# Performance work log

Measured on AMD Instinct MI355X. Metric: run time of the kernel, lower is better.

Reference implementation:

```python
import jax, jax.numpy as jnp
import numpy as np

LATENT_CH = 64  # feature_ch // 8


def conv1x1(x, w):
    # Conv2dLayer with kernel_size=1, bias=False, activation='linear':
    # weight_gain = 1/sqrt(in_channels * 1)
    gain = 1.0 / np.sqrt(w.shape[1])
    return jnp.einsum('bchw,oc->bohw', x, w * gain)


def casual_attention(q, k, v):
    # q,k,v: [B, C, N] / [B, C, M]; score = q^T k, softmax over keys, out = score @ v^T
    score = jnp.einsum('bcn,bcm->bnm', q, k)
    score = jax.nn.softmax(score, axis=-1)
    return jnp.einsum('bnm,bcm->bnc', score, v)  # [B, N, C]


def reference(feature_map, concepts, w_theta, w_phi, w_g, w_o, gamma_sa, gamma_moca):
    B, C, H, W = feature_map.shape
    L = LATENT_CH
    HW = H * W

    # ---- SelfAttention ----
    th = conv1x1(feature_map, w_theta).reshape(B, L, HW)
    ph = conv1x1(feature_map, w_phi).reshape(B, L, HW)
    g = conv1x1(feature_map, w_g).reshape(B, L, HW)
    # torch does .view(-1, L, H, W) on a [B, HW, L] tensor -> raw memory reinterpret
    lat = casual_attention(th, ph, g).reshape(B, L, H, W)
    sa_out = gamma_sa * conv1x1(lat, w_o) + feature_map

    # ---- MomentumConceptAttention (theta and o shared with SA, trainable_conv=False) ----
    enc = conv1x1(sa_out, w_theta).reshape(B, L, HW)
    phi_c = concepts.T[None]                      # [1, L, P]  (torch.no_grad on concepts)
    phi_c = jnp.broadcast_to(phi_c, (B, L, concepts.shape[0]))
    lat2 = casual_attention(enc, phi_c, phi_c).reshape(B, L, H, W)
    out = gamma_moca * conv1x1(lat2, w_o) + sa_out
    return out


def setup_inputs() -> dict:
    key = jax.random.key(0)
    ks = jax.random.split(key, 8)
    B, C, H, W = 8, 512, 64, 64
    L, P = LATENT_CH, 256
    return {
        'feature_map': jax.random.normal(ks[0], (B, C, H, W), jnp.float32),
        'concepts': jax.random.normal(ks[1], (P, L), jnp.float32),
        'w_theta': jax.random.normal(ks[2], (L, C), jnp.float32),
        'w_phi': jax.random.normal(ks[3], (L, C), jnp.float32),
        'w_g': jax.random.normal(ks[4], (L, C), jnp.float32),
        'w_o': jax.random.normal(ks[5], (C, L), jnp.float32),
        'gamma_sa': jnp.float32(0.1),
        'gamma_moca': jnp.float32(0.1),
    }
```

## Files before the change

### kernel.cpp

```cpp
#include <hip/hip_runtime.h>
#include <math.h>

#define HW   4096
#define CINP 512
#define LCH  64

typedef short bf8 __attribute__((ext_vector_type(8)));
typedef float f4  __attribute__((ext_vector_type(4)));
typedef unsigned int u32x2 __attribute__((ext_vector_type(2)));

__device__ __forceinline__ unsigned short f2bf(float x) {
    union { float f; unsigned int u; } v; v.f = x;
    return (unsigned short)((v.u + 0x7fffu + ((v.u >> 16) & 1u)) >> 16);
}
__device__ __forceinline__ bf8 ldbf8(const unsigned short* p) {
    uint4 u = *(const uint4*)p;
    return __builtin_bit_cast(bf8, u);
}
__device__ __forceinline__ unsigned int cvtpk(float a, float b) {
    unsigned int r;
    asm volatile("v_cvt_pk_bf16_f32 %0, %1, %2" : "=v"(r) : "v"(a), "v"(b));
    return r;
}

__global__ __launch_bounds__(256) void precast(
    const float* __restrict__ wt, const float* __restrict__ wp,
    const float* __restrict__ wg, const float* __restrict__ wo,
    const float* __restrict__ conc,
    unsigned short* __restrict__ WB, unsigned short* __restrict__ WO,
    unsigned short* __restrict__ CK, unsigned short* __restrict__ CV)
{
    const float gain = 0.04419417382415922f;
    int id = blockIdx.x * 256 + threadIdx.x;
    if (id < 98304) {
        int o = id >> 9, k = id & 511;
        const float* w = (o < 64) ? wt : (o < 128) ? wp : wg;
        WB[id] = f2bf(w[(o & 63) * 512 + k] * gain);
    } else if (id < 131072) {
        int j = id - 98304;
        WO[j] = f2bf(wo[j]);
    } else if (id < 147456) {
        int j = id - 131072;
        CK[j] = f2bf(conc[j]);
    } else if (id < 163840) {
        int j = id - 147456;
        int l = j >> 8, m = j & 255;
        CV[j] = f2bf(conc[m * 64 + l]);
    }
}

__global__ __launch_bounds__(256) void cast_transpose(const float* __restrict__ x,
                                                      unsigned short* __restrict__ XT)
{
    __shared__ unsigned short Lb[64][72];
    const int t  = threadIdx.x;
    const int n0 = blockIdx.x * 64, c0 = blockIdx.y * 64, b = blockIdx.z;
    const float* xb = x + ((size_t)b * CINP + c0) * HW + n0;
    const int cc = t >> 4, n4 = (t & 15) * 4;
    #pragma unroll
    for (int i = 0; i < 4; i++) {
        int c = cc + i * 16;
        float4 v = *(const float4*)(xb + (size_t)c * HW + n4);
        Lb[n4 + 0][c] = f2bf(v.x);
        Lb[n4 + 1][c] = f2bf(v.y);
        Lb[n4 + 2][c] = f2bf(v.z);
        Lb[n4 + 3][c] = f2bf(v.w);
    }
    __syncthreads();
    const int n = t & 63, cb0 = t >> 6;
    unsigned short* orow = XT + ((size_t)b * HW + n0 + n) * CINP + c0;
    #pragma unroll
    for (int i = 0; i < 2; i++) {
        int cb = cb0 + i * 4;
        *(uint4*)(orow + cb * 8) = *(const uint4*)&Lb[n][cb * 8];
    }
}

__global__ __launch_bounds__(256) void lat_transpose(const unsigned short* __restrict__ A,
                                                     unsigned short* __restrict__ LT)
{
    __shared__ unsigned short Ls[64][72];
    const int t = threadIdx.x, s0 = blockIdx.x * 64, b = blockIdx.y;
    const unsigned short* ab = A + (size_t)b * LCH * HW;
    #pragma unroll
    for (int it = 0; it < 2; it++) {
        int c = (t >> 3) + it * 32, s8 = (t & 7) * 8;
        union { uint4 u; unsigned short s[8]; } v;
        v.u = *(const uint4*)(ab + (size_t)c * HW + s0 + s8);
        #pragma unroll
        for (int i = 0; i < 8; i++) Ls[s8 + i][c] = v.s[i];
    }
    __syncthreads();
    unsigned short* ob = LT + ((size_t)b * HW + s0) * LCH;
    #pragma unroll
    for (int it = 0; it < 2; it++) {
        int s = (t >> 3) + it * 32, c8 = (t & 7);
        *(uint4*)(ob + (size_t)s * LCH + c8 * 8) = *(const uint4*)&Ls[s][c8 * 8];
    }
}

template <int NRT>
__global__ __launch_bounds__(256) void qkv_gemm(unsigned short* XT,
                                                const unsigned short* __restrict__ WB,
                                                unsigned short* __restrict__ VL)
{
    const int t = threadIdx.x;
    const int wave = t >> 6, lane = t & 63, quad = lane >> 4, lidx = lane & 15;
    const int b = blockIdx.y;
    const int ncol = blockIdx.x * 64 + wave * 16 + lidx;
    unsigned short* xrow = XT + ((size_t)b * HW + ncol) * CINP;

    f4 acc[NRT];
    #pragma unroll
    for (int r = 0; r < NRT; r++) acc[r] = (f4){0.f, 0.f, 0.f, 0.f};

    for (int kk = 0; kk < 16; kk++) {
        const int k0 = kk * 32 + quad * 8;
        bf8 bq = ldbf8(xrow + k0);
        #pragma unroll
        for (int rt = 0; rt < NRT; rt++) {
            bf8 aw = ldbf8(WB + (size_t)(rt * 16 + lidx) * CINP + k0);
            acc[rt] = __builtin_amdgcn_mfma_f32_16x16x32_bf16(aw, bq, acc[rt], 0, 0, 0);
        }
    }

    #pragma unroll
    for (int rt = 0; rt < NRT; rt++) {
        if (rt < 8) {
            union { unsigned short s[4]; uint2 u; } pk;
            #pragma unroll
            for (int r = 0; r < 4; r++) pk.s[r] = f2bf(acc[rt][r]);
            int off = (rt < 4) ? (rt * 16 + quad * 4) : (64 + (rt - 4) * 16 + quad * 4);
            *(uint2*)(xrow + off) = pk.u;
        } else {
            #pragma unroll
            for (int r = 0; r < 4; r++) {
                int l = (rt - 8) * 16 + quad * 4 + r;
                VL[((size_t)b * LCH + l) * HW + ncol] = f2bf(acc[rt][r]);
            }
        }
    }
}

__global__ __launch_bounds__(128) void flash(
    const unsigned short* Qb, size_t qbat,
    const unsigned short* Kb, size_t krow, size_t kbat,
    const unsigned short* Vb, size_t vrow, size_t vbat,
    unsigned short* __restrict__ Aout, int nkeys)
{
    __shared__ __align__(16) unsigned short Ks[2][32][72];
    __shared__ __align__(16) unsigned short Vs[2][64][40];

    const int t = threadIdx.x;
    const int wave = t >> 6, lane = t & 63, quad = lane >> 4, lidx = lane & 15;
    const int b = blockIdx.y, q0 = blockIdx.x * 64 + wave * 32;

    const unsigned short* qp = Qb + (size_t)b * qbat;
    const unsigned short* kp = Kb + (size_t)b * kbat;
    const unsigned short* vp = Vb + (size_t)b * vbat;

    const int kkey0 = t >> 3, kch = t & 7;
    const int kkey1 = kkey0 + 16;
    const int vr0 = t >> 2, vch = t & 3;
    const int vr1 = vr0 + 32;

    bf8 qa[2][2];
    #pragma unroll
    for (int qb = 0; qb < 2; qb++)
        #pragma unroll
        for (int kh = 0; kh < 2; kh++)
            qa[qb][kh] = ldbf8(qp + (size_t)(q0 + qb * 16 + lidx) * CINP + kh * 32 + quad * 8);

    f4 O[2][4];
    float Lp[2] = {0.f, 0.f};
    #pragma unroll
    for (int qb = 0; qb < 2; qb++)
        #pragma unroll
        for (int lt = 0; lt < 4; lt++) O[qb][lt] = (f4){0.f, 0.f, 0.f, 0.f};

    const int nt = nkeys >> 5;

    {
        uint4 k0 = *(const uint4*)(kp + (size_t)kkey0 * krow + kch * 8);
        uint4 k1 = *(const uint4*)(kp + (size_t)kkey1 * krow + kch * 8);
        uint4 v0 = *(const uint4*)(vp + (size_t)vr0 * vrow + vch * 8);
        uint4 v1 = *(const uint4*)(vp + (size_t)vr1 * vrow + vch * 8);
        *(uint4*)&Ks[0][kkey0][kch * 8] = k0;
        *(uint4*)&Ks[0][kkey1][kch * 8] = k1;
        *(uint4*)&Vs[0][vr0][vch * 8] = v0;
        *(uint4*)&Vs[0][vr1][vch * 8] = v1;
    }
    __syncthreads();

    for (int tl = 0; tl < nt; tl++) {
        const int cur = tl & 1;
        const bool pfv = (tl + 1 < nt);
        uint4 kq0, kq1, vq0, vq1;
        if (pfv) {
            const int m1 = (tl + 1) * 32;
            kq0 = *(const uint4*)(kp + (size_t)(m1 + kkey0) * krow + kch * 8);
            kq1 = *(const uint4*)(kp + (size_t)(m1 + kkey1) * krow + kch * 8);
            vq0 = *(const uint4*)(vp + (size_t)vr0 * vrow + m1 + vch * 8);
            vq1 = *(const uint4*)(vp + (size_t)vr1 * vrow + m1 + vch * 8);
        }

        bf8 kf[2][2];
        #pragma unroll
        for (int ms = 0; ms < 2; ms++)
            #pragma unroll
            for (int kh = 0; kh < 2; kh++)
                kf[ms][kh] = *(const bf8*)&Ks[cur][ms * 16 + lidx][kh * 32 + quad * 8];

        f4 S[2][2];
        #pragma unroll
        for (int qb = 0; qb < 2; qb++)
            #pragma unroll
            for (int ms = 0; ms < 2; ms++) {
                f4 s = (f4){0.f, 0.f, 0.f, 0.f};
                s = __builtin_amdgcn_mfma_f32_16x16x32_bf16(kf[ms][0], qa[qb][0], s, 0, 0, 0);
                s = __builtin_amdgcn_mfma_f32_16x16x32_bf16(kf[ms][1], qa[qb][1], s, 0, 0, 0);
                S[qb][ms] = s;
            }

        bf8 pa[2];
        #pragma unroll
        for (int qb = 0; qb < 2; qb++) {
            float e00 = __expf(S[qb][0][0]), e01 = __expf(S[qb][0][1]);
            float e02 = __expf(S[qb][0][2]), e03 = __expf(S[qb][0][3]);
            float e10 = __expf(S[qb][1][0]), e11 = __expf(S[qb][1][1]);
            float e12 = __expf(S[qb][1][2]), e13 = __expf(S[qb][1][3]);
            Lp[qb] += ((e00 + e01) + (e02 + e03)) + ((e10 + e11) + (e12 + e13));
            unsigned int A = cvtpk(e00, e01), B = cvtpk(e02, e03);
            unsigned int C = cvtpk(e10, e11), D = cvtpk(e12, e13);
            u32x2 ac = __builtin_amdgcn_permlane32_swap(A, C, false, false);
            u32x2 xz = __builtin_amdgcn_permlane16_swap(ac.x, ac.y, false, false);
            u32x2 bd = __builtin_amdgcn_permlane32_swap(B, D, false, false);
            u32x2 yw = __builtin_amdgcn_permlane16_swap(bd.x, bd.y, false, false);
            uint4 pu; pu.x = xz.x; pu.y = yw.x; pu.z = xz.y; pu.w = yw.y;
            pa[qb] = __builtin_bit_cast(bf8, pu);
        }

        #pragma unroll
        for (int lt = 0; lt < 4; lt++) {
            bf8 vf = *(const bf8*)&Vs[cur][lt * 16 + lidx][quad * 8];
            O[0][lt] = __builtin_amdgcn_mfma_f32_16x16x32_bf16(pa[0], vf, O[0][lt], 0, 0, 0);
            O[1][lt] = __builtin_amdgcn_mfma_f32_16x16x32_bf16(pa[1], vf, O[1][lt], 0, 0, 0);
        }

        if (pfv) {
            *(uint4*)&Ks[cur ^ 1][kkey0][kch * 8] = kq0;
            *(uint4*)&Ks[cur ^ 1][kkey1][kch * 8] = kq1;
            *(uint4*)&Vs[cur ^ 1][vr0][vch * 8] = vq0;
            *(uint4*)&Vs[cur ^ 1][vr1][vch * 8] = vq1;
        }
        __syncthreads();
    }

    float inv[2];
    #pragma unroll
    for (int qb = 0; qb < 2; qb++) {
        float s = Lp[qb];
        s += __shfl_xor(s, 16);
        s += __shfl_xor(s, 32);
        inv[qb] = 1.f / s;
    }
    #pragma unroll
    for (int qb = 0; qb < 2; qb++)
        #pragma unroll
        for (int r = 0; r < 4; r++) {
            float iv = __shfl(inv[qb], quad * 4 + r);
            size_t n = (size_t)b * HW + q0 + qb * 16 + quad * 4 + r;
            #pragma unroll
            for (int lt = 0; lt < 4; lt++)
                Aout[n * LCH + lt * 16 + lidx] = f2bf(O[qb][lt][r] * iv);
        }
}

__global__ __launch_bounds__(256) void conv_o(const unsigned short* __restrict__ LT,
                                              const unsigned short* __restrict__ WO,
                                              const float* __restrict__ res,
                                              const float* __restrict__ gamma_p,
                                              float* __restrict__ out,
                                              unsigned short* ST)
{
    const int t = threadIdx.x;
    const int wave = t >> 6, lane = t & 63, quad = lane >> 4, lidx = lane & 15;
    const int b = blockIdx.z, o0 = blockIdx.y * 64;
    const int scol = blockIdx.x * 64 + wave * 16 + lidx;
    const unsigned short* arow = LT + ((size_t)b * HW + scol) * LCH;

    f4 acc[4];
    #pragma unroll
    for (int ot = 0; ot < 4; ot++) acc[ot] = (f4){0.f, 0.f, 0.f, 0.f};

    #pragma unroll
    for (int kh = 0; kh < 2; kh++) {
        bf8 bq = ldbf8(arow + kh * 32 + quad * 8);
        #pragma unroll
        for (int ot = 0; ot < 4; ot++) {
            bf8 af = ldbf8(WO + (size_t)(o0 + ot * 16 + lidx) * LCH + kh * 32 + quad * 8);
            acc[ot] = __builtin_amdgcn_mfma_f32_16x16x32_bf16(af, bq, acc[ot], 0, 0, 0);
        }
    }

    const float scale = gamma_p[0] * 0.125f;
    #pragma unroll
    for (int ot = 0; ot < 4; ot++) {
        float v[4];
        #pragma unroll
        for (int r = 0; r < 4; r++) {
            size_t idx = ((size_t)b * CINP + o0 + ot * 16 + quad * 4 + r) * HW + scol;
            v[r] = fmaf(scale, acc[ot][r], res[idx]);
            out[idx] = v[r];
        }
        if (ST) {
            union { unsigned short s[4]; uint2 u; } pk;
            #pragma unroll
            for (int r = 0; r < 4; r++) pk.s[r] = f2bf(v[r]);
            *(uint2*)(ST + ((size_t)b * HW + scol) * CINP + o0 + ot * 16 + quad * 4) = pk.u;
        }
    }
}

extern "C" void kernel_launch(void* const* d_in, const int* in_sizes, int n_in,
                              void* d_out, int out_size, void* d_ws, size_t ws_size,
                              hipStream_t stream)
{
    const float* f    = (const float*)d_in[0];
    const float* conc = (const float*)d_in[1];
    const float* wt   = (const float*)d_in[2];
    const float* wp   = (const float*)d_in[3];
    const float* wg   = (const float*)d_in[4];
    const float* wo   = (const float*)d_in[5];
    const float* gsa  = (const float*)d_in[6];
    const float* gmo  = (const float*)d_in[7];
    float* out = (float*)d_out;

    char* ws = (char*)d_ws;
    unsigned short* XT = (unsigned short*)ws;
    unsigned short* VL = (unsigned short*)(ws + ((size_t)32 << 20));
    unsigned short* LT = VL;
    unsigned short* A1 = (unsigned short*)(ws + ((size_t)36 << 20));
    unsigned short* WB = (unsigned short*)(ws + ((size_t)40 << 20));
    unsigned short* WO = WB + 192 * 512;
    unsigned short* CK = WO + 512 * 64;
    unsigned short* CV = CK + 256 * 64;

    dim3 blk256(256), blk128(128);

    precast<<<640, blk256, 0, stream>>>(wt, wp, wg, wo, conc, WB, WO, CK, CV);
    cast_transpose<<<dim3(64, 8, 8), blk256, 0, stream>>>(f, XT);

    qkv_gemm<12><<<dim3(64, 8), blk256, 0, stream>>>(XT, WB, VL);
    flash<<<dim3(64, 8), blk128, 0, stream>>>(
        XT, (size_t)HW * CINP,
        XT + 64, CINP, (size_t)HW * CINP,
        VL, HW, (size_t)LCH * HW,
        A1, HW);
    lat_transpose<<<dim3(64, 8), blk256, 0, stream>>>(A1, LT);
    conv_o<<<dim3(64, 8, 8), blk256, 0, stream>>>(LT, WO, f, gsa, out, XT );

    qkv_gemm<4><<<dim3(64, 8), blk256, 0, stream>>>(XT , WB , nullptr);
    flash<<<dim3(64, 8), blk128, 0, stream>>>(
        XT, (size_t)HW * CINP,
        CK, LCH, 0,
        CV, 256, 0,
        A1 , 256);
    lat_transpose<<<dim3(64, 8), blk256, 0, stream>>>(A1, LT);
    conv_o<<<dim3(64, 8, 8), blk256, 0, stream>>>(LT, WO, out, gmo, out, nullptr);
}
```

Measured before the change: 399.9 us.

## Split flash attention keys across two wave groups with LDS reduction

Flash blocks grow to 512 threads covering 128 queries. Two groups of four waves each take half of every 64-key tile, then combine partial outputs and row sums through shared memory before normalising. The aim is to load each K/V tile once for twice as many queries and to add more waves per block. In exchange there is an extra LDS reduction and barrier at the end, and half the waves sit idle during the output write.

```diff
diff --git a/kernel.cpp b/kernel.cpp
--- a/kernel.cpp
+++ b/kernel.cpp
@@ -142,27 +142,31 @@
     }
 }
 
-__global__ __launch_bounds__(128) void flash(
+__global__ __launch_bounds__(512) void flash(
     const unsigned short* Qb, size_t qbat,
     const unsigned short* Kb, size_t krow, size_t kbat,
     const unsigned short* Vb, size_t vrow, size_t vbat,
     unsigned short* __restrict__ Aout, int nkeys)
 {
-    __shared__ __align__(16) unsigned short Ks[2][32][72];
-    __shared__ __align__(16) unsigned short Vs[2][64][40];
+    __shared__ __align__(16) char smem[38912];
+    unsigned short (*Ks)[64][72]     = (unsigned short (*)[64][72])smem;
+    unsigned short (*Vs)[2][64][40]  = (unsigned short (*)[2][64][40])(smem + 18432);
+    float* Red = (float*)smem;
 
     const int t = threadIdx.x;
     const int wave = t >> 6, lane = t & 63, quad = lane >> 4, lidx = lane & 15;
-    const int b = blockIdx.y, q0 = blockIdx.x * 64 + wave * 32;
+    const int qh = wave & 3, g = wave >> 2;
+    const int b = blockIdx.y, q0 = blockIdx.x * 128 + qh * 32;
 
     const unsigned short* qp = Qb + (size_t)b * qbat;
     const unsigned short* kp = Kb + (size_t)b * kbat;
     const unsigned short* vp = Vb + (size_t)b * vbat;
 
-    const int kkey0 = t >> 3, kch = t & 7;
-    const int kkey1 = kkey0 + 16;
-    const int vr0 = t >> 2, vch = t & 3;
-    const int vr1 = vr0 + 32;
+    const int srow = t >> 3, sch = t & 7;
+    const int vseg = sch >> 2, vcs = sch & 3;
+    const unsigned short* ksrc = kp + (size_t)srow * krow + sch * 8;
+    const unsigned short* vsrc = vp + (size_t)srow * vrow + sch * 8;
+    const size_t kstep = (size_t)64 * krow;
 
     bf8 qa[2][2];
     #pragma unroll
@@ -178,30 +182,21 @@
         #pragma unroll
         for (int lt = 0; lt < 4; lt++) O[qb][lt] = (f4){0.f, 0.f, 0.f, 0.f};
 
-    const int nt = nkeys >> 5;
-
-    {
-        uint4 k0 = *(const uint4*)(kp + (size_t)kkey0 * krow + kch * 8);
-        uint4 k1 = *(const uint4*)(kp + (size_t)kkey1 * krow + kch * 8);
-        uint4 v0 = *(const uint4*)(vp + (size_t)vr0 * vrow + vch * 8);
-        uint4 v1 = *(const uint4*)(vp + (size_t)vr1 * vrow + vch * 8);
-        *(uint4*)&Ks[0][kkey0][kch * 8] = k0;
-        *(uint4*)&Ks[0][kkey1][kch * 8] = k1;
-        *(uint4*)&Vs[0][vr0][vch * 8] = v0;
-        *(uint4*)&Vs[0][vr1][vch * 8] = v1;
-    }
+    const int nt = nkeys >> 6;
+
+    *(uint4*)&Ks[0][srow][sch * 8]       = *(const uint4*)ksrc;
+    *(uint4*)&Vs[0][vseg][srow][vcs * 8] = *(const uint4*)vsrc;
+    ksrc += kstep; vsrc += 64;
     __syncthreads();
 
     for (int tl = 0; tl < nt; tl++) {
         const int cur = tl & 1;
         const bool pfv = (tl + 1 < nt);
-        uint4 kq0, kq1, vq0, vq1;
+        uint4 kq, vq;
         if (pfv) {
-            const int m1 = (tl + 1) * 32;
-            kq0 = *(const uint4*)(kp + (size_t)(m1 + kkey0) * krow + kch * 8);
-            kq1 = *(const uint4*)(kp + (size_t)(m1 + kkey1) * krow + kch * 8);
-            vq0 = *(const uint4*)(vp + (size_t)vr0 * vrow + m1 + vch * 8);
-            vq1 = *(const uint4*)(vp + (size_t)vr1 * vrow + m1 + vch * 8);
+            kq = *(const uint4*)ksrc;
+            vq = *(const uint4*)vsrc;
+            ksrc += kstep; vsrc += 64;
         }
 
         bf8 kf[2][2];
@@ -209,7 +204,7 @@
         for (int ms = 0; ms < 2; ms++)
             #pragma unroll
             for (int kh = 0; kh < 2; kh++)
-                kf[ms][kh] = *(const bf8*)&Ks[cur][ms * 16 + lidx][kh * 32 + quad * 8];
+                kf[ms][kh] = *(const bf8*)&Ks[cur][g * 32 + ms * 16 + lidx][kh * 32 + quad * 8];
 
         f4 S[2][2];
         #pragma unroll
@@ -242,38 +237,62 @@
 
         #pragma unroll
         for (int lt = 0; lt < 4; lt++) {
-            bf8 vf = *(const bf8*)&Vs[cur][lt * 16 + lidx][quad * 8];
+            bf8 vf = *(const bf8*)&Vs[cur][g][lt * 16 + lidx][quad * 8];
             O[0][lt] = __builtin_amdgcn_mfma_f32_16x16x32_bf16(pa[0], vf, O[0][lt], 0, 0, 0);
             O[1][lt] = __builtin_amdgcn_mfma_f32_16x16x32_bf16(pa[1], vf, O[1][lt], 0, 0, 0);
         }
 
         if (pfv) {
-            *(uint4*)&Ks[cur ^ 1][kkey0][kch * 8] = kq0;
-            *(uint4*)&Ks[cur ^ 1][kkey1][kch * 8] = kq1;
-            *(uint4*)&Vs[cur ^ 1][vr0][vch * 8] = vq0;
-            *(uint4*)&Vs[cur ^ 1][vr1][vch * 8] = vq1;
+            *(uint4*)&Ks[cur ^ 1][srow][sch * 8]       = kq;
+            *(uint4*)&Vs[cur ^ 1][vseg][srow][vcs * 8] = vq;
         }
         __syncthreads();
     }
 
-    float inv[2];
-    #pragma unroll
-    for (int qb = 0; qb < 2; qb++) {
-        float s = Lp[qb];
-        s += __shfl_xor(s, 16);
-        s += __shfl_xor(s, 32);
-        inv[qb] = 1.f / s;
-    }
-    #pragma unroll
-    for (int qb = 0; qb < 2; qb++)
-        #pragma unroll
-        for (int r = 0; r < 4; r++) {
-            float iv = __shfl(inv[qb], quad * 4 + r);
-            size_t n = (size_t)b * HW + q0 + qb * 16 + quad * 4 + r;
+    if (g == 1) {
+        float* rp = Red + (size_t)(qh * 64 + lane) * 35;
+        int j = 0;
+        #pragma unroll
+        for (int qb = 0; qb < 2; qb++)
             #pragma unroll
             for (int lt = 0; lt < 4; lt++)
-                Aout[n * LCH + lt * 16 + lidx] = f2bf(O[qb][lt][r] * iv);
-        }
+                #pragma unroll
+                for (int r = 0; r < 4; r++) rp[j++] = O[qb][lt][r];
+        rp[32] = Lp[0];
+        rp[33] = Lp[1];
+    }
+    __syncthreads();
+    if (g == 0) {
+        const float* rp = Red + (size_t)(qh * 64 + lane) * 35;
+        int j = 0;
+        #pragma unroll
+        for (int qb = 0; qb < 2; qb++)
+            #pragma unroll
+            for (int lt = 0; lt < 4; lt++)
+                #pragma unroll
+                for (int r = 0; r < 4; r++) O[qb][lt][r] += rp[j++];
+        Lp[0] += rp[32];
+        Lp[1] += rp[33];
+
+        float inv[2];
+        #pragma unroll
+        for (int qb = 0; qb < 2; qb++) {
+            float s = Lp[qb];
+            s += __shfl_xor(s, 16);
+            s += __shfl_xor(s, 32);
+            inv[qb] = 1.f / s;
+        }
+        #pragma unroll
+        for (int qb = 0; qb < 2; qb++)
+            #pragma unroll
+            for (int r = 0; r < 4; r++) {
+                float iv = __shfl(inv[qb], quad * 4 + r);
+                size_t n = (size_t)b * HW + q0 + qb * 16 + quad * 4 + r;
+                #pragma unroll
+                for (int lt = 0; lt < 4; lt++)
+                    Aout[n * LCH + lt * 16 + lidx] = f2bf(O[qb][lt][r] * iv);
+            }
+    }
 }
 
 __global__ __launch_bounds__(256) void conv_o(const unsigned short* __restrict__ LT,
@@ -346,13 +365,13 @@
     unsigned short* CK = WO + 512 * 64;
     unsigned short* CV = CK + 256 * 64;
 
-    dim3 blk256(256), blk128(128);
+    dim3 blk256(256), blk512(512);
 
     precast<<<640, blk256, 0, stream>>>(wt, wp, wg, wo, conc, WB, WO, CK, CV);
     cast_transpose<<<dim3(64, 8, 8), blk256, 0, stream>>>(f, XT);
 
     qkv_gemm<12><<<dim3(64, 8), blk256, 0, stream>>>(XT, WB, VL);
-    flash<<<dim3(64, 8), blk128, 0, stream>>>(
+    flash<<<dim3(32, 8), blk512, 0, stream>>>(
         XT, (size_t)HW * CINP,
         XT + 64, CINP, (size_t)HW * CINP,
         VL, HW, (size_t)LCH * HW,
@@ -361,7 +380,7 @@
     conv_o<<<dim3(64, 8, 8), blk256, 0, stream>>>(LT, WO, f, gsa, out, XT );
 
     qkv_gemm<4><<<dim3(64, 8), blk256, 0, stream>>>(XT , WB , nullptr);
-    flash<<<dim3(64, 8), blk128, 0, stream>>>(
+    flash<<<dim3(32, 8), blk512, 0, stream>>>(
         XT, (size_t)HW * CINP,
         CK, LCH, 0,
         CV, 256, 0,
```

After: 356.8 us. -10.8%, faster.
